# Kernel optimization log

Measured on AMD Instinct MI355X. Metric: run time of the kernel, lower is better.

The kernel has to match this reference:

```python
import jax, jax.numpy as jnp
import numpy as np

N = 100000   # nodes
E = 1600000  # edges
IN_DIM, HID, HEADS, OUT_DIM = 8, 64, 4, 3


def _add_self_loops(src, dst, n):
    loop = jnp.arange(n, dtype=src.dtype)
    return jnp.concatenate([src, loop]), jnp.concatenate([dst, loop])


def gcn_conv(x, src, dst, n, W, b):
    # PyG GCNConv: add self-loops, symmetric normalization deg^-1/2 * deg^-1/2
    s, d = _add_self_loops(src, dst, n)
    deg = jax.ops.segment_sum(jnp.ones(s.shape[0], x.dtype), d, num_segments=n)
    dinv = jnp.where(deg > 0, jax.lax.rsqrt(deg), 0.0)
    norm = dinv[s] * dinv[d]                       # [E']
    h = x @ W                                      # [N, out]
    out = jax.ops.segment_sum(norm[:, None] * h[s], d, num_segments=n)
    return out + b


def gat_conv(x, src, dst, n, W, att_src, att_dst, b):
    # PyG GATConv, concat=True, negative_slope=0.2, self-loops added
    h = (x @ W).reshape(n, HEADS, HID)             # [N, H, C]
    s, d = _add_self_loops(src, dst, n)
    a_src = jnp.sum(h * att_src, axis=-1)          # [N, H]
    a_dst = jnp.sum(h * att_dst, axis=-1)          # [N, H]
    e = jax.nn.leaky_relu(a_src[s] + a_dst[d], negative_slope=0.2)  # [E', H]
    m = jax.lax.stop_gradient(jax.ops.segment_max(e, d, num_segments=n))
    ex = jnp.exp(e - m[d])
    denom = jax.ops.segment_sum(ex, d, num_segments=n)
    alpha = ex / (denom[d] + 1e-16)                # segment softmax over incoming edges
    out = jax.ops.segment_sum(alpha[:, :, None] * h[s], d, num_segments=n)  # [N, H, C]
    return out.reshape(n, HEADS * HID) + b


def setup_inputs() -> dict:
    key = jax.random.key(0)
    ks = jax.random.split(key, 16)
    def glorot(k, shape):
        fan = shape[0] + shape[-1]
        return jax.random.normal(k, shape, jnp.float32) * np.sqrt(2.0 / fan)
    return {
        "x": jax.random.normal(ks[0], (N, IN_DIM), jnp.float32),
        "edge_index": jax.random.randint(ks[1], (2, E), 0, N, jnp.int64 if jax.config.jax_enable_x64 else jnp.int32),
        "w1": glorot(ks[2], (IN_DIM, HID)), "b1": jnp.zeros((HID,), jnp.float32),
        "w2": glorot(ks[3], (HID, HID)),   "b2": jnp.zeros((HID,), jnp.float32),
        "w3": glorot(ks[4], (HID, HID)),   "b3": jnp.zeros((HID,), jnp.float32),
        "wg": glorot(ks[5], (HID, HEADS * HID)), "bg": jnp.zeros((HEADS * HID,), jnp.float32),
        "att_src": glorot(ks[6], (HEADS, HID)),
        "att_dst": glorot(ks[7], (HEADS, HID)),
        "wc1": glorot(ks[8], (HEADS * HID, HID)), "bc1": jnp.zeros((HID,), jnp.float32),
        "wc2": glorot(ks[9], (HID, OUT_DIM)),     "bc2": jnp.zeros((OUT_DIM,), jnp.float32),
    }


def reference(x, edge_index, w1, b1, w2, b2, w3, b3, wg, bg, att_src, att_dst, wc1, bc1, wc2, bc2):
    src, dst = edge_index[0], edge_index[1]
    n = x.shape[0]
    # stacked GCN convs with ReLU; residual when shapes match (layers 2,3)
    h = jax.nn.relu(gcn_conv(x, src, dst, n, w1, b1))
    h = h + jax.nn.relu(gcn_conv(h, src, dst, n, w2, b2))
    h = h + jax.nn.relu(gcn_conv(h, src, dst, n, w3, b3))
    # GAT attention layer (4 heads, concat)
    h_att = gat_conv(h, src, dst, n, wg, att_src, att_dst, bg)  # [N, 256]
    # classifier MLP (dropout is inference no-op)
    z = jax.nn.relu(h_att @ wc1 + bc1)
    logits = z @ wc2 + bc2
    return jax.nn.log_softmax(logits, axis=1)
```

## Files before the change

### kernel.cpp

```cpp
#include <hip/hip_runtime.h>
#include <math.h>


typedef _Float16 half8 __attribute__((ext_vector_type(8)));
typedef _Float16 half2v __attribute__((ext_vector_type(2)));

__device__ __forceinline__ float leaky02(float v) { return v > 0.f ? v : 0.2f * v; }


template <int CTRL>
__device__ __forceinline__ float dpp_add(float v) {
    int iv = __builtin_bit_cast(int, v);
    int r = __builtin_amdgcn_update_dpp(iv, iv, CTRL, 0xF, 0xF, false);
    return v + __builtin_bit_cast(float, r);
}
template <int OFF>
__device__ __forceinline__ float swz_add(float v) {
    int r = __builtin_amdgcn_ds_swizzle(__builtin_bit_cast(int, v), OFF);
    return v + __builtin_bit_cast(float, r);
}
__device__ __forceinline__ float red8(float v) {
    v = dpp_add<0xB1>(v);
    v = dpp_add<0x4E>(v);
    v = swz_add<0x101F>(v);
    return v;
}
__device__ __forceinline__ float red64(float v) {
    v = dpp_add<0xB1>(v);
    v = dpp_add<0x4E>(v);
    v = swz_add<0x101F>(v);
    v = dpp_add<0x128>(v);
    v = swz_add<0x401F>(v);
    v = v + __shfl_xor(v, 32);
    return v;
}
__device__ __forceinline__ float sel4(int g, float v0, float v1, float v2, float v3) {
    return g == 0 ? v0 : g == 1 ? v1 : g == 2 ? v2 : v3;
}


__global__ void count_kernel(const int* __restrict__ dst, int E, int range,
                             int* __restrict__ counts) {
    int grp = blockIdx.x & 7;
    int nlo = grp * range;
    int nhi = nlo + range;
    int nblk = gridDim.x >> 3;
    int c = blockIdx.x >> 3;
    int stride = nblk * blockDim.x;
    for (int e = c * blockDim.x + threadIdx.x; e < E; e += stride) {
        int d = dst[e];
        if (d >= nlo && d < nhi) atomicAdd(&counts[d], 1);
    }
}

__global__ void scan_pass1(const int* __restrict__ counts, int n, int* __restrict__ blockSums) {
    __shared__ int sh[256];
    int base = blockIdx.x * 2048;
    int tid = threadIdx.x;
    int s = 0;
#pragma unroll
    for (int j = 0; j < 8; ++j) {
        int idx = base + tid * 8 + j;
        if (idx < n) s += counts[idx];
    }
    sh[tid] = s;
    __syncthreads();
    for (int off = 128; off > 0; off >>= 1) {
        if (tid < off) sh[tid] += sh[tid + off];
        __syncthreads();
    }
    if (tid == 0) blockSums[blockIdx.x] = sh[0];
}

__global__ void scan_pass2(const int* __restrict__ blockSums, int nb, int* __restrict__ blockOffs) {
    if (threadIdx.x == 0 && blockIdx.x == 0) {
        int run = 0;
        for (int i = 0; i < nb; ++i) { blockOffs[i] = run; run += blockSums[i]; }
    }
}

__global__ void scan_pass3(const int* __restrict__ counts, int n,
                           const int* __restrict__ blockOffs,
                           const float* __restrict__ x,
                           int* __restrict__ row_ptr, int* __restrict__ cursor,
                           float* __restrict__ dinv, float* __restrict__ rdinv,
                           _Float16* __restrict__ xs) {
    __shared__ int sh[256];
    int base = blockIdx.x * 2048;
    int tid = threadIdx.x;
    int cnt[8];
    int local = 0;
#pragma unroll
    for (int j = 0; j < 8; ++j) {
        int idx = base + tid * 8 + j;
        cnt[j] = (idx < n) ? counts[idx] : 0;
        local += cnt[j];
    }
    sh[tid] = local;
    __syncthreads();
    for (int off = 1; off < 256; off <<= 1) {
        int v = (tid >= off) ? sh[tid - off] : 0;
        __syncthreads();
        sh[tid] += v;
        __syncthreads();
    }
    int run = blockOffs[blockIdx.x] + sh[tid] - local;
#pragma unroll
    for (int j = 0; j < 8; ++j) {
        int idx = base + tid * 8 + j;
        if (idx < n) {
            row_ptr[idx] = run;
            cursor[idx] = run;
            float dv = rsqrtf((float)(cnt[j] + 1));
            dinv[idx] = dv;
            rdinv[idx] = sqrtf((float)(cnt[j] + 1));
#pragma unroll
            for (int t = 0; t < 8; ++t) xs[idx * 8 + t] = (_Float16)(dv * x[idx * 8 + t]);
            run += cnt[j];
            if (idx == n - 1) row_ptr[n] = run;
        }
    }
}

__global__ void scatter_kernel(const int* __restrict__ src, const int* __restrict__ dst,
                               int E, int range,
                               int* __restrict__ cursor, int* __restrict__ col_src) {
    int grp = blockIdx.x & 7;
    int nlo = grp * range;
    int nhi = nlo + range;
    int nblk = gridDim.x >> 3;
    int c = blockIdx.x >> 3;
    int stride = nblk * blockDim.x;
    for (int e = c * blockDim.x + threadIdx.x; e < E; e += stride) {
        int d = dst[e];
        if (d >= nlo && d < nhi) {
            int pos = atomicAdd(&cursor[d], 1);
            col_src[pos] = src[e];
        }
    }
}


__global__ void ccomb_kernel(const float* __restrict__ Wg, const float* __restrict__ bg,
                             const float* __restrict__ wc1, const float* __restrict__ bc1,
                             const float* __restrict__ att_src, const float* __restrict__ att_dst,
                             float* __restrict__ Ccomb, float* __restrict__ bcomb,
                             float* __restrict__ wse, float* __restrict__ wde) {
    int bid = blockIdx.x;
    int j = threadIdx.x;
    if (bid < 256) {
        int h = bid >> 6, k = bid & 63;
        float s = 0.f;
        for (int c = 0; c < 64; ++c)
            s += Wg[k * 256 + h * 64 + c] * wc1[(h * 64 + c) * 64 + j];
        Ccomb[bid * 64 + j] = s;
    } else {
        float s = bc1[j];
        for (int i = 0; i < 256; ++i) s += bg[i] * wc1[i * 64 + j];
        bcomb[j] = s;
#pragma unroll
        for (int h = 0; h < 4; ++h) {
            float ss = 0.f, sd = 0.f;
            for (int c = 0; c < 64; ++c) {
                float w = Wg[j * 256 + h * 64 + c];
                ss += w * att_src[h * 64 + c];
                sd += w * att_dst[h * 64 + c];
            }
            wse[j * 4 + h] = ss;
            wde[j * 4 + h] = sd;
        }
    }
}


__global__ void gcn_layer1(const half8* __restrict__ xs8,
                           const float* __restrict__ W1, const float* __restrict__ b1,
                           const int* __restrict__ row_ptr, const int* __restrict__ col_src,
                           const float* __restrict__ dinv, int n,
                           _Float16* __restrict__ hs1) {
    int tid = threadIdx.x, lane = tid & 63, wid = tid >> 6;
    int node = blockIdx.x * 4 + wid;
    if (node >= n) return;
    int beg = row_ptr[node], end = row_ptr[node + 1];
    int deg = end - beg;
    float acc[8] = {0.f, 0.f, 0.f, 0.f, 0.f, 0.f, 0.f, 0.f};
    for (int base = 0; base < deg; base += 64) {
        int cs = col_src[min(beg + base + lane, end - 1)];
        half8 v = xs8[cs];
        if (base + lane < deg) {
#pragma unroll
            for (int c = 0; c < 8; ++c) acc[c] += (float)v[c];
        }
    }
#pragma unroll
    for (int c = 0; c < 8; ++c) acc[c] = red64(acc[c]);
    half8 sv = xs8[node];
    float di = dinv[node];
    float agg[8];
#pragma unroll
    for (int c = 0; c < 8; ++c) agg[c] = (acc[c] + (float)sv[c]) * di;
    float sum = b1[lane];
#pragma unroll
    for (int k = 0; k < 8; ++k) sum = fmaf(agg[k], W1[k * 64 + lane], sum);
    hs1[node * 64 + lane] = (_Float16)(di * fmaxf(sum, 0.f));
}


template <bool LAST>
__global__ void gcn_layer64(const _Float16* __restrict__ hs_in,
                            const float* __restrict__ W, const float* __restrict__ b,
                            const int* __restrict__ row_ptr, const int* __restrict__ col_src,
                            const float* __restrict__ dinv, const float* __restrict__ rdinv,
                            const float* __restrict__ wse, const float* __restrict__ wde,
                            int n,
                            _Float16* __restrict__ hout,
                            float4* __restrict__ a_src4, float4* __restrict__ a_dst4) {
    __shared__ float agg_lds[4][64];
    int tid = threadIdx.x;
    int lane = tid & 63;
    int wid = tid >> 6;
    int t = lane >> 3, g = lane & 7;
    const half8* hs8 = (const half8*)hs_in;
    float wreg[64];
#pragma unroll
    for (int k = 0; k < 64; ++k) wreg[k] = W[k * 64 + lane];
    float bl = b[lane];
    float4 we, wd;
    if (LAST) {
        we = ((const float4*)wse)[lane];
        wd = ((const float4*)wde)[lane];
    }
    int nw = gridDim.x * 4;
    for (int node = blockIdx.x * 4 + wid; node < n; node += nw) {
        int beg = row_ptr[node], end = row_ptr[node + 1];
        int deg = end - beg;
        half8 sv = hs8[node * 8 + t];
        float ac[8];
#pragma unroll
        for (int c = 0; c < 8; ++c) ac[c] = (g == 0) ? (float)sv[c] : 0.f;
        for (int base = 0; base < deg; base += 64) {
            int cs = col_src[min(beg + base + lane, end - 1)];
            int lim = min(deg - base, 64);
            auto bodyF = [&](int eo8) {
                int s = __shfl(cs, eo8 + g);
                half8 v = hs8[s * 8 + t];
#pragma unroll
                for (int c = 0; c < 8; ++c) ac[c] += (float)v[c];
            };
            auto bodyG = [&](int eo8) {
                int eo = eo8 + g;
                int s = __shfl(cs, eo);
                half8 v = hs8[s * 8 + t];
                if (eo < lim) {
#pragma unroll
                    for (int c = 0; c < 8; ++c) ac[c] += (float)v[c];
                }
            };
            int eo8 = 0;
            for (; eo8 + 16 <= lim; eo8 += 16) { bodyF(eo8); bodyF(eo8 + 8); }
            if (eo8 < lim) {
                bodyG(eo8);
                eo8 += 8;
                if (eo8 < lim) bodyG(eo8);
            }
        }
        float di = dinv[node];
#pragma unroll
        for (int c = 0; c < 8; ++c) ac[c] = red8(ac[c]) * di;
        if (g == 0) {
            *(float4*)&agg_lds[wid][t * 8]     = make_float4(ac[0], ac[1], ac[2], ac[3]);
            *(float4*)&agg_lds[wid][t * 8 + 4] = make_float4(ac[4], ac[5], ac[6], ac[7]);
        }
        __asm__ volatile("s_waitcnt lgkmcnt(0)" ::: "memory");
        float sum = bl;
#pragma unroll
        for (int k4 = 0; k4 < 16; ++k4) {
            float4 a4 = *(const float4*)&agg_lds[wid][k4 * 4];
            sum = fmaf(a4.x, wreg[k4 * 4 + 0], sum);
            sum = fmaf(a4.y, wreg[k4 * 4 + 1], sum);
            sum = fmaf(a4.z, wreg[k4 * 4 + 2], sum);
            sum = fmaf(a4.w, wreg[k4 * 4 + 3], sum);
        }
        float hprev = rdinv[node] * (float)sv[g];
        float hv = hprev + fmaxf(sum, 0.f);
        if (!LAST) {
            hout[node * 64 + lane] = (_Float16)(di * hv);
        } else {
            hout[node * 64 + lane] = (_Float16)hv;
            float vs0 = red64(hv * we.x), vs1 = red64(hv * we.y);
            float vs2 = red64(hv * we.z), vs3 = red64(hv * we.w);
            float vd0 = red64(hv * wd.x), vd1 = red64(hv * wd.y);
            float vd2 = red64(hv * wd.z), vd3 = red64(hv * wd.w);
            if (lane == 0) {
                a_src4[node] = make_float4(vs0, vs1, vs2, vs3);
                a_dst4[node] = make_float4(vd0, vd1, vd2, vd3);
            }
        }
    }
}


__global__ void gat_agg(const _Float16* __restrict__ h3,
                        const float4* __restrict__ a_src4, const float4* __restrict__ a_dst4,
                        const int* __restrict__ row_ptr, const int* __restrict__ col_src,
                        int n, _Float16* __restrict__ aggout) {
    __shared__ float4 w_lds[4][64];
    __shared__ int    s_lds[4][64];
    int tid = threadIdx.x, lane = tid & 63, wid = tid >> 6;
    int node = blockIdx.x * 4 + wid;
    if (node >= n) return;
    int t = lane >> 3, g = lane & 7;
    const half8* h38 = (const half8*)h3;

    float4 ad = a_dst4[node];
    half8 hself = h38[node * 8 + t];
    float A[4][8], dh[4];
    {
        float4 asf = a_src4[node];
        float w0 = __expf(leaky02(asf.x + ad.x));
        float w1 = __expf(leaky02(asf.y + ad.y));
        float w2 = __expf(leaky02(asf.z + ad.z));
        float w3 = __expf(leaky02(asf.w + ad.w));
        float m0 = (g == 0) ? 1.f : 0.f;
        dh[0] = m0 * w0; dh[1] = m0 * w1; dh[2] = m0 * w2; dh[3] = m0 * w3;
#pragma unroll
        for (int c = 0; c < 8; ++c) {
            float hvc = (float)hself[c];
            A[0][c] = dh[0] * hvc;
            A[1][c] = dh[1] * hvc;
            A[2][c] = dh[2] * hvc;
            A[3][c] = dh[3] * hvc;
        }
    }
    int beg = row_ptr[node], end = row_ptr[node + 1];
    int deg = end - beg;
    for (int base = 0; base < deg; base += 64) {
        int cs = col_src[min(beg + base + lane, end - 1)];
        float4 as = a_src4[cs];
        float valid = (base + lane < deg) ? 1.f : 0.f;
        float4 wv;
        wv.x = valid * __expf(leaky02(as.x + ad.x));
        wv.y = valid * __expf(leaky02(as.y + ad.y));
        wv.z = valid * __expf(leaky02(as.z + ad.z));
        wv.w = valid * __expf(leaky02(as.w + ad.w));
        w_lds[wid][lane] = wv;
        s_lds[wid][lane] = cs;
        __asm__ volatile("s_waitcnt lgkmcnt(0)" ::: "memory");
        int lim = min(deg - base, 64);
        auto body = [&](int eo8) {
            int eo = eo8 + g;
            int s = s_lds[wid][eo];
            float4 w4 = w_lds[wid][eo];
            half8 hv = h38[s * 8 + t];
#pragma unroll
            for (int c = 0; c < 8; ++c) {
                float hvc = (float)hv[c];
                A[0][c] = fmaf(w4.x, hvc, A[0][c]);
                A[1][c] = fmaf(w4.y, hvc, A[1][c]);
                A[2][c] = fmaf(w4.z, hvc, A[2][c]);
                A[3][c] = fmaf(w4.w, hvc, A[3][c]);
            }
            dh[0] += w4.x; dh[1] += w4.y; dh[2] += w4.z; dh[3] += w4.w;
        };
        int eo8 = 0;
        for (; eo8 + 16 <= lim; eo8 += 16) { body(eo8); body(eo8 + 8); }
        if (eo8 < lim) {
            body(eo8);
            eo8 += 8;
            if (eo8 < lim) body(eo8);
        }
    }
#pragma unroll
    for (int h = 0; h < 4; ++h) {
#pragma unroll
        for (int c = 0; c < 8; ++c) A[h][c] = red8(A[h][c]);
        dh[h] = red8(dh[h]);
    }
    float r0 = 1.f / (dh[0] + 1e-16f);
    float r1 = 1.f / (dh[1] + 1e-16f);
    float r2 = 1.f / (dh[2] + 1e-16f);
    float r3 = 1.f / (dh[3] + 1e-16f);
    if (g < 4) {
        float r = sel4(g, r0, r1, r2, r3);
        half8 hv;
#pragma unroll
        for (int c = 0; c < 8; ++c)
            hv[c] = (_Float16)(sel4(g, A[0][c], A[1][c], A[2][c], A[3][c]) * r);
        *(half8*)(aggout + (size_t)node * 256 + g * 64 + t * 8) = hv;
    }
}


__global__ __launch_bounds__(256) void mlp_kernel(
        const _Float16* __restrict__ agg,
        const float* __restrict__ Ccomb, const float* __restrict__ bcomb,
        const float* __restrict__ wc2, const float* __restrict__ bc2,
        int n, float* __restrict__ out) {
    __shared__ float part[4][4][64];
    int tid = threadIdx.x;
    int lane = tid & 63;
    int w = __builtin_amdgcn_readfirstlane(tid >> 6);
    float creg[64];
#pragma unroll
    for (int i = 0; i < 64; ++i) creg[i] = Ccomb[(w * 64 + i) * 64 + lane];
    float bz = bcomb[lane];
    float w20 = wc2[lane * 3 + 0], w21 = wc2[lane * 3 + 1], w22 = wc2[lane * 3 + 2];
    float bb0 = bc2[0], bb1 = bc2[1], bb2 = bc2[2];
    int nchunks = (n + 3) >> 2;
    for (int ch = blockIdx.x; ch < nchunks; ch += gridDim.x) {
        int base = ch * 4;
#pragma unroll
        for (int j = 0; j < 4; ++j) {
            int li = min(base + j, n - 1);
            const half2v* a2 = (const half2v*)(agg + (size_t)li * 256 + w * 64);
            float p = 0.f;
#pragma unroll
            for (int i = 0; i < 32; ++i) {
                half2v hv = a2[i];
                p = fmaf((float)hv[0], creg[2 * i], p);
                p = fmaf((float)hv[1], creg[2 * i + 1], p);
            }
            part[j][w][lane] = p;
        }
        __syncthreads();
        int li = base + w;
        if (li < n) {
            float z = bz + part[w][0][lane] + part[w][1][lane]
                         + part[w][2][lane] + part[w][3][lane];
            z = fmaxf(z, 0.f);
            float p0 = red64(z * w20);
            float p1 = red64(z * w21);
            float p2 = red64(z * w22);
            if (lane == 0) {
                float e0 = p0 + bb0, e1 = p1 + bb1, e2 = p2 + bb2;
                float mx = fmaxf(e0, fmaxf(e1, e2));
                float lse = mx + logf(expf(e0 - mx) + expf(e1 - mx) + expf(e2 - mx));
                out[li * 3 + 0] = e0 - lse;
                out[li * 3 + 1] = e1 - lse;
                out[li * 3 + 2] = e2 - lse;
            }
        }
        __syncthreads();
    }
}


extern "C" void kernel_launch(void* const* d_in, const int* in_sizes, int n_in,
                              void* d_out, int out_size, void* d_ws, size_t ws_size,
                              hipStream_t stream) {
    const float* x       = (const float*)d_in[0];
    const int*   ei      = (const int*)d_in[1];
    const float* w1      = (const float*)d_in[2];
    const float* b1      = (const float*)d_in[3];
    const float* w2      = (const float*)d_in[4];
    const float* b2      = (const float*)d_in[5];
    const float* w3      = (const float*)d_in[6];
    const float* b3      = (const float*)d_in[7];
    const float* wg      = (const float*)d_in[8];
    const float* bg      = (const float*)d_in[9];
    const float* att_s   = (const float*)d_in[10];
    const float* att_d   = (const float*)d_in[11];
    const float* wc1     = (const float*)d_in[12];
    const float* bc1     = (const float*)d_in[13];
    const float* wc2     = (const float*)d_in[14];
    const float* bc2     = (const float*)d_in[15];
    float* out = (float*)d_out;

    const int N = in_sizes[0] / 8;
    const int E = in_sizes[1] / 2;
    const int* srcv = ei;
    const int* dstv = ei + E;

    char* ws = (char*)d_ws;
    size_t off = 0;
    auto alloc = [&](size_t bytes) -> char* {
        char* p = ws + off;
        off += (bytes + 255) & ~(size_t)255;
        return p;
    };
    int*      counts    = (int*)alloc((size_t)N * 4);
    int*      row_ptr   = (int*)alloc((size_t)(N + 1) * 4);
    int*      cursor    = (int*)alloc((size_t)N * 4);
    int*      col_src   = (int*)alloc((size_t)E * 4);
    int*      blockSums = (int*)alloc(4096 * 4);
    int*      blockOffs = (int*)alloc(4096 * 4);
    float*    dinv      = (float*)alloc((size_t)N * 4);
    float*    rdinv     = (float*)alloc((size_t)N * 4);
    _Float16* xs        = (_Float16*)alloc((size_t)N * 8 * 2);
    float*    a_src     = (float*)alloc((size_t)N * 16);
    float*    a_dst     = (float*)alloc((size_t)N * 16);
    float*    wse       = (float*)alloc(256 * 4);
    float*    wde       = (float*)alloc(256 * 4);
    float*    Ccomb     = (float*)alloc(256 * 64 * 4);
    float*    bcomb     = (float*)alloc(64 * 4);
    _Float16* bufA      = (_Float16*)alloc((size_t)N * 64 * 2);
    _Float16* bufB      = (_Float16*)alloc((size_t)N * 64 * 2);
    _Float16* aggbuf    = (_Float16*)alloc((size_t)N * 256 * 2);
    _Float16* hs1 = bufA;
    _Float16* hs2 = bufB;
    _Float16* h3  = bufA;
    (void)ws_size; (void)n_in; (void)out_size;

    hipMemsetAsync(counts, 0, (size_t)N * 4, stream);

    const int TPB = 256;
    int range = (N + 7) / 8;
    count_kernel<<<1024, TPB, 0, stream>>>(dstv, E, range, counts);

    int NB = (N + 2047) / 2048;
    scan_pass1<<<NB, TPB, 0, stream>>>(counts, N, blockSums);
    scan_pass2<<<1, 64, 0, stream>>>(blockSums, NB, blockOffs);
    scan_pass3<<<NB, TPB, 0, stream>>>(counts, N, blockOffs, x,
                                       row_ptr, cursor, dinv, rdinv, xs);
    scatter_kernel<<<2048, TPB, 0, stream>>>(srcv, dstv, E, range, cursor, col_src);

    ccomb_kernel<<<257, 64, 0, stream>>>(wg, bg, wc1, bc1, att_s, att_d,
                                         Ccomb, bcomb, wse, wde);

    int gridN = (N + 3) / 4;
    gcn_layer1<<<gridN, TPB, 0, stream>>>((const half8*)xs, w1, b1, row_ptr, col_src,
                                          dinv, N, hs1);
    const int G64 = 2048;
    gcn_layer64<false><<<G64, TPB, 0, stream>>>(hs1, w2, b2, row_ptr, col_src,
                                                dinv, rdinv, wse, wde, N, hs2,
                                                nullptr, nullptr);
    gcn_layer64<true><<<G64, TPB, 0, stream>>>(hs2, w3, b3, row_ptr, col_src,
                                               dinv, rdinv, wse, wde, N, h3,
                                               (float4*)a_src, (float4*)a_dst);

    gat_agg<<<gridN, TPB, 0, stream>>>(h3, (const float4*)a_src, (const float4*)a_dst,
                                       row_ptr, col_src, N, aggbuf);
    mlp_kernel<<<1024, TPB, 0, stream>>>(aggbuf, Ccomb, bcomb, wc2, bc2, N, out);
}
```

Baseline: 625.9 us.

## Compute classifier MLP with MFMA using split-fp16 pre-packed weights

Replaces the scalar FMA classifier kernel with one using 16x16x32 fp16 MFMA instructions over 16-node tiles. The combined weight matrix is pre-packed by the ccomb kernel into the MFMA B-operand layout, stored as hi/lo fp16 pairs so accuracy stays near fp32. Each wave computes 16 output columns, and results are reduced through small shared-memory partials. The goal is to cut VALU work and per-thread register-resident weights in the final dense layer, at the cost of twice the MFMA count and extra layout complexity.

```diff
diff --git a/kernel.cpp b/kernel.cpp
--- a/kernel.cpp
+++ b/kernel.cpp
@@ -3,7 +3,8 @@
 
 
 typedef _Float16 half8 __attribute__((ext_vector_type(8)));
-typedef _Float16 half2v __attribute__((ext_vector_type(2)));
+typedef _Float16 f16x8 __attribute__((ext_vector_type(8)));
+typedef float f32x4 __attribute__((ext_vector_type(4)));
 
 __device__ __forceinline__ float leaky02(float v) { return v > 0.f ? v : 0.2f * v; }
 
@@ -23,6 +24,13 @@
     v = dpp_add<0xB1>(v);
     v = dpp_add<0x4E>(v);
     v = swz_add<0x101F>(v);
+    return v;
+}
+__device__ __forceinline__ float red16(float v) {
+    v = dpp_add<0xB1>(v);
+    v = dpp_add<0x4E>(v);
+    v = swz_add<0x101F>(v);
+    v = dpp_add<0x128>(v);
     return v;
 }
 __device__ __forceinline__ float red64(float v) {
@@ -144,16 +152,20 @@
 __global__ void ccomb_kernel(const float* __restrict__ Wg, const float* __restrict__ bg,
                              const float* __restrict__ wc1, const float* __restrict__ bc1,
                              const float* __restrict__ att_src, const float* __restrict__ att_dst,
-                             float* __restrict__ Ccomb, float* __restrict__ bcomb,
+                             _Float16* __restrict__ CcombP, float* __restrict__ bcomb,
                              float* __restrict__ wse, float* __restrict__ wde) {
     int bid = blockIdx.x;
     int j = threadIdx.x;
     if (bid < 256) {
-        int h = bid >> 6, k = bid & 63;
+        int i = bid;
         float s = 0.f;
         for (int c = 0; c < 64; ++c)
-            s += Wg[k * 256 + h * 64 + c] * wc1[(h * 64 + c) * 64 + j];
-        Ccomb[bid * 64 + j] = s;
+            s += Wg[(i & 63) * 256 + (i >> 6) * 64 + c] * wc1[((i >> 6) * 64 + c) * 64 + j];
+        _Float16 hi = (_Float16)s;
+        _Float16 lo = (_Float16)(s - (float)hi);
+        int kt = i >> 5, l = (((i >> 3) & 3) << 4) | (j & 15), e = i & 7, ct = j >> 4;
+        CcombP[(ct * 8 + kt) * 512 + l * 8 + e] = hi;
+        CcombP[(32 + ct * 8 + kt) * 512 + l * 8 + e] = lo;
     } else {
         float s = bc1[j];
         for (int i = 0; i < 256; ++i) s += bg[i] * wc1[i * 64 + j];
@@ -391,53 +403,71 @@
 }
 
 
-__global__ __launch_bounds__(256) void mlp_kernel(
+__global__ __launch_bounds__(256) void mlp_mfma(
         const _Float16* __restrict__ agg,
-        const float* __restrict__ Ccomb, const float* __restrict__ bcomb,
+        const _Float16* __restrict__ CP,
+        const float* __restrict__ bcomb,
         const float* __restrict__ wc2, const float* __restrict__ bc2,
         int n, float* __restrict__ out) {
-    __shared__ float part[4][4][64];
+    __shared__ float part[4][16][3];
     int tid = threadIdx.x;
     int lane = tid & 63;
     int w = __builtin_amdgcn_readfirstlane(tid >> 6);
-    float creg[64];
-#pragma unroll
-    for (int i = 0; i < 64; ++i) creg[i] = Ccomb[(w * 64 + i) * 64 + lane];
-    float bz = bcomb[lane];
-    float w20 = wc2[lane * 3 + 0], w21 = wc2[lane * 3 + 1], w22 = wc2[lane * 3 + 2];
+    int c16 = lane & 15, hi = lane >> 4;
+
+    f16x8 bh[8], blo[8];
+#pragma unroll
+    for (int kt = 0; kt < 8; ++kt) {
+        bh[kt]  = *(const f16x8*)(CP + (size_t)(w * 8 + kt) * 512 + lane * 8);
+        blo[kt] = *(const f16x8*)(CP + (size_t)(32 + w * 8 + kt) * 512 + lane * 8);
+    }
+    int col = w * 16 + c16;
+    float bc  = bcomb[col];
+    float w20 = wc2[col * 3 + 0], w21 = wc2[col * 3 + 1], w22 = wc2[col * 3 + 2];
     float bb0 = bc2[0], bb1 = bc2[1], bb2 = bc2[2];
-    int nchunks = (n + 3) >> 2;
-    for (int ch = blockIdx.x; ch < nchunks; ch += gridDim.x) {
-        int base = ch * 4;
-#pragma unroll
-        for (int j = 0; j < 4; ++j) {
-            int li = min(base + j, n - 1);
-            const half2v* a2 = (const half2v*)(agg + (size_t)li * 256 + w * 64);
-            float p = 0.f;
-#pragma unroll
-            for (int i = 0; i < 32; ++i) {
-                half2v hv = a2[i];
-                p = fmaf((float)hv[0], creg[2 * i], p);
-                p = fmaf((float)hv[1], creg[2 * i + 1], p);
+
+    int ntiles = (n + 15) >> 4;
+    for (int tile = blockIdx.x; tile < ntiles; tile += gridDim.x) {
+        int rowb = tile * 16;
+        int row = min(rowb + c16, n - 1);
+        const _Float16* ap = agg + (size_t)row * 256 + hi * 8;
+        f16x8 a[8];
+#pragma unroll
+        for (int kt = 0; kt < 8; ++kt) a[kt] = *(const f16x8*)(ap + kt * 32);
+        f32x4 acc = {0.f, 0.f, 0.f, 0.f};
+#pragma unroll
+        for (int kt = 0; kt < 8; ++kt) {
+            acc = __builtin_amdgcn_mfma_f32_16x16x32_f16(a[kt], bh[kt],  acc, 0, 0, 0);
+            acc = __builtin_amdgcn_mfma_f32_16x16x32_f16(a[kt], blo[kt], acc, 0, 0, 0);
+        }
+        float pr[4][3];
+#pragma unroll
+        for (int r = 0; r < 4; ++r) {
+            float z = fmaxf(acc[r] + bc, 0.f);
+            pr[r][0] = red16(z * w20);
+            pr[r][1] = red16(z * w21);
+            pr[r][2] = red16(z * w22);
+        }
+        if (c16 == 0) {
+#pragma unroll
+            for (int r = 0; r < 4; ++r) {
+                part[w][hi * 4 + r][0] = pr[r][0];
+                part[w][hi * 4 + r][1] = pr[r][1];
+                part[w][hi * 4 + r][2] = pr[r][2];
             }
-            part[j][w][lane] = p;
         }
         __syncthreads();
-        int li = base + w;
-        if (li < n) {
-            float z = bz + part[w][0][lane] + part[w][1][lane]
-                         + part[w][2][lane] + part[w][3][lane];
-            z = fmaxf(z, 0.f);
-            float p0 = red64(z * w20);
-            float p1 = red64(z * w21);
-            float p2 = red64(z * w22);
-            if (lane == 0) {
-                float e0 = p0 + bb0, e1 = p1 + bb1, e2 = p2 + bb2;
+        if (tid < 16) {
+            int node = rowb + tid;
+            if (node < n) {
+                float e0 = part[0][tid][0] + part[1][tid][0] + part[2][tid][0] + part[3][tid][0] + bb0;
+                float e1 = part[0][tid][1] + part[1][tid][1] + part[2][tid][1] + part[3][tid][1] + bb1;
+                float e2 = part[0][tid][2] + part[1][tid][2] + part[2][tid][2] + part[3][tid][2] + bb2;
                 float mx = fmaxf(e0, fmaxf(e1, e2));
                 float lse = mx + logf(expf(e0 - mx) + expf(e1 - mx) + expf(e2 - mx));
-                out[li * 3 + 0] = e0 - lse;
-                out[li * 3 + 1] = e1 - lse;
-                out[li * 3 + 2] = e2 - lse;
+                out[(size_t)node * 3 + 0] = e0 - lse;
+                out[(size_t)node * 3 + 1] = e1 - lse;
+                out[(size_t)node * 3 + 2] = e2 - lse;
             }
         }
         __syncthreads();
@@ -491,7 +521,7 @@
     float*    a_dst     = (float*)alloc((size_t)N * 16);
     float*    wse       = (float*)alloc(256 * 4);
     float*    wde       = (float*)alloc(256 * 4);
-    float*    Ccomb     = (float*)alloc(256 * 64 * 4);
+    _Float16* CcombP    = (_Float16*)alloc(64 * 1024);
     float*    bcomb     = (float*)alloc(64 * 4);
     _Float16* bufA      = (_Float16*)alloc((size_t)N * 64 * 2);
     _Float16* bufB      = (_Float16*)alloc((size_t)N * 64 * 2);
@@ -515,7 +545,7 @@
     scatter_kernel<<<2048, TPB, 0, stream>>>(srcv, dstv, E, range, cursor, col_src);
 
     ccomb_kernel<<<257, 64, 0, stream>>>(wg, bg, wc1, bc1, att_s, att_d,
-                                         Ccomb, bcomb, wse, wde);
+                                         CcombP, bcomb, wse, wde);
 
     int gridN = (N + 3) / 4;
     gcn_layer1<<<gridN, TPB, 0, stream>>>((const half8*)xs, w1, b1, row_ptr, col_src,
@@ -530,5 +560,5 @@
 
     gat_agg<<<gridN, TPB, 0, stream>>>(h3, (const float4*)a_src, (const float4*)a_dst,
                                        row_ptr, col_src, N, aggbuf);
-    mlp_kernel<<<1024, TPB, 0, stream>>>(aggbuf, Ccomb, bcomb, wc2, bc2, N, out);
-}
+    mlp_mfma<<<2048, TPB, 0, stream>>>(aggbuf, CcombP, bcomb, wc2, bc2, N, out);
+}
```

After: 560.4 us. 1.12x faster.
